# Kernel tuning notes

Hardware: AMD Instinct MI355X
Metric: run time of the kernel (lower is better)

The kernel has to match this reference:

```python
import jax, jax.numpy as jnp
import numpy as np

B, L, C, NEC = 1, 256, 1024, 2000


def setup_inputs() -> dict:
    key = jax.random.key(0)
    ks = jax.random.split(key, 8)
    attentions = jax.random.normal(ks[0], (B, L, C), jnp.float32)
    pooled = jax.random.normal(ks[1], (B, C), jnp.float32)
    attention_mask = jax.random.randint(ks[2], (B, L), 0, 2).astype(jnp.int32)
    lin1_w = jax.random.normal(ks[3], (C, C), jnp.float32) * 0.02
    lin1_b = jnp.zeros((C,), jnp.float32)
    cls_w = jax.random.normal(ks[4], (NEC, C), jnp.float32) * 0.02
    cls_b = jnp.zeros((NEC,), jnp.float32)
    conv1_w = jax.random.normal(ks[5], (C, 2 * C), jnp.float32) * 0.02  # 1x1 conv as matrix
    conv1_b = jnp.zeros((C,), jnp.float32)
    w2 = jax.random.normal(ks[6], (1, C, 7, 7), jnp.float32) * 0.02
    conv2_w = 0.5 * (w2 + jnp.swapaxes(w2, 2, 3))  # clip(): symmetrize kernel
    conv2_b = jnp.zeros((1,), jnp.float32)
    return dict(attentions=attentions, pooled=pooled, attention_mask=attention_mask,
                lin1_w=lin1_w, lin1_b=lin1_b, cls_w=cls_w, cls_b=cls_b,
                conv1_w=conv1_w, conv1_b=conv1_b, conv2_w=conv2_w, conv2_b=conv2_b)


def reference(attentions, pooled, attention_mask, lin1_w, lin1_b, cls_w, cls_b,
              conv1_w, conv1_b, conv2_w, conv2_b):
    # EC-classification head (dropout is identity at inference)
    logits = (pooled @ lin1_w.T + lin1_b) @ cls_w.T + cls_b  # [B, NEC]

    # mask out [CLS] (pos 0) and [SEP] (pos = sum of mask)
    s = attention_mask.sum(axis=1)
    mask = attention_mask.at[jnp.arange(B), s].set(0).at[:, 0].set(0)
    z = attentions * mask[:, :, None].astype(attentions.dtype)  # [B, L, C]
    z = jnp.swapaxes(z, 1, 2)                                   # [B, C, L]

    # pairwise |zi - zj| and zi * zj -> [B, 2C, L, L]
    z_diff = jnp.abs(z[:, :, None, :] - z[:, :, :, None])
    z_mul = z[:, :, None, :] * z[:, :, :, None]
    feat = jnp.concatenate([z_diff, z_mul], axis=1)

    # 1x1 conv (channel contraction) + ReLU
    h = jax.nn.relu(jnp.einsum('oc,bcij->boij', conv1_w, feat)
                    + conv1_b[None, :, None, None])            # [B, C, L, L]

    # 7x7 conv, padding 3, symmetric kernel, sigmoid
    out = jax.lax.conv_general_dilated(
        h, conv2_w, window_strides=(1, 1), padding=[(3, 3), (3, 3)],
        dimension_numbers=('NCHW', 'OIHW', 'NCHW')) + conv2_b[None, :, None, None]
    maps = jax.nn.sigmoid(out)                                  # [B, 1, L, L]
    return logits, maps.reshape(-1, L * L)
```

## Files before the change

### kernel.cpp

```cpp
#include <hip/hip_runtime.h>

typedef float  f4v    __attribute__((ext_vector_type(4)));
typedef __bf16 bf16x8 __attribute__((ext_vector_type(8)));
typedef __bf16 bf16x4 __attribute__((ext_vector_type(4)));

#define PCAP  16384
#define LDQ   16384
#define CH    1024
#define KI    2048
#define KIT   32

__device__ __forceinline__ int offA(int r, int A) { return r * A - ((r * (r - 1)) >> 1); }

__device__ __forceinline__ int mask_scan(const int* am, int t, int* act,
                                         unsigned long long* wm, int* wred) {
    int wave = t >> 6, lane = t & 63;
    int a = am[t];
    int sv = a;
#pragma unroll
    for (int d = 32; d; d >>= 1) sv += __shfl_down(sv, d);
    if (lane == 0) wred[wave] = sv;
    __syncthreads();
    int s = wred[0] + wred[1] + wred[2] + wred[3];
    int keep = (t != 0 && t != s && a != 0) ? 1 : 0;
    unsigned long long bm = __ballot(keep);
    if (lane == 0) wm[wave] = bm;
    __syncthreads();
    int base = 0, A = 0;
#pragma unroll
    for (int w = 0; w < 4; w++) {
        int pc = __popcll(wm[w]);
        if (w < wave) base += pc;
        A += pc;
    }
    if (keep) act[base + __popcll(bm & ((1ull << lane) - 1ull))] = t;
    __syncthreads();
    return A;
}

#define PB_FEATP  0
#define PB_FEATS  2048
#define PB_CVTA   2080
#define PB_K2     2592
#define PB_QCONST 2848
#define PB_ZERO   2897
#define PB_SCAN   3694
#define PB_HID    3695
#define PB_TOTAL  3951

__global__ void k_prep(const float* __restrict__ att, const int* __restrict__ am,
                       const float* __restrict__ c1w, const float* __restrict__ c2w,
                       const float* __restrict__ c1b,
                       const float* __restrict__ pooled, const float* __restrict__ lin1_w,
                       const float* __restrict__ lin1_b,
                       int* rank, int* counts, __bf16* featT, __bf16* A1p, __bf16* K2w,
                       float* Qc, float* Qzero, float* hid) {
    int b = blockIdx.x, t = threadIdx.x;

    if (b < PB_FEATS) {
        __shared__ int act[256];
        __shared__ unsigned long long wm[4];
        __shared__ int wred[4];
        int A = mask_scan(am, t, act, wm, wred);
        int P = (A * (A + 1)) >> 1;
        int Ppad = ((P + 127) >> 7) << 7;
        if (Ppad > PCAP) { Ppad = PCAP; P = PCAP; }
        int n0 = b * 8;
        if (n0 >= Ppad) return;
        int c0 = t * 4;
        float fA = (float)(2 * A + 1);
        for (int q = 0; q < 8; q++) {
            int n = n0 + q;
            bf16x8 ov;
            if (n < P && A > 0) {
                float disc = fmaxf(fA * fA - 8.0f * (float)n, 0.0f);
                int r = (int)floorf((fA - sqrtf(disc)) * 0.5f);
                r = min(A - 1, max(0, r));
                while (r > 0 && offA(r, A) > n) --r;
                while (r < A - 1 && offA(r + 1, A) <= n) ++r;
                int i = act[r], j = act[r + (n - offA(r, A))];
                float4 a = *(const float4*)&att[i * CH + c0];
                float4 bj = *(const float4*)&att[j * CH + c0];
                ov[0] = (__bf16)fabsf(a.x - bj.x); ov[1] = (__bf16)(a.x * bj.x);
                ov[2] = (__bf16)fabsf(a.y - bj.y); ov[3] = (__bf16)(a.y * bj.y);
                ov[4] = (__bf16)fabsf(a.z - bj.z); ov[5] = (__bf16)(a.z * bj.z);
                ov[6] = (__bf16)fabsf(a.w - bj.w); ov[7] = (__bf16)(a.w * bj.w);
            } else {
#pragma unroll
                for (int r8 = 0; r8 < 8; r8++) ov[r8] = (__bf16)0.0f;
            }
            *(bf16x8*)&featT[(size_t)n * KI + t * 8] = ov;
        }
    } else if (b < PB_CVTA) {
        int r0 = (b - PB_FEATS) * 8;
        int c0 = t * 4;
        for (int q = 0; q < 8; q++) {
            int r = r0 + q;
            float4 a = *(const float4*)&att[r * CH + c0];
            bf16x8 ov;
            ov[0] = (__bf16)fabsf(a.x); ov[1] = (__bf16)0.f;
            ov[2] = (__bf16)fabsf(a.y); ov[3] = (__bf16)0.f;
            ov[4] = (__bf16)fabsf(a.z); ov[5] = (__bf16)0.f;
            ov[6] = (__bf16)fabsf(a.w); ov[7] = (__bf16)0.f;
            *(bf16x8*)&featT[(size_t)(PCAP + r) * KI + t * 8] = ov;
        }
    } else if (b < PB_K2) {
        int gid = (b - PB_CVTA) * 256 + t;
        int o = gid >> 7, cw = (gid & 127) * 8;
        const float* wd = &c1w[o * 2048 + cw];
        const float* wmu = &c1w[o * 2048 + 1024 + cw];
        float4 d0 = *(const float4*)wd,  d1 = *(const float4*)(wd + 4);
        float4 m0 = *(const float4*)wmu, m1 = *(const float4*)(wmu + 4);
        bf16x8 v0, v1;
        v0[0] = (__bf16)d0.x; v0[1] = (__bf16)m0.x; v0[2] = (__bf16)d0.y; v0[3] = (__bf16)m0.y;
        v0[4] = (__bf16)d0.z; v0[5] = (__bf16)m0.z; v0[6] = (__bf16)d0.w; v0[7] = (__bf16)m0.w;
        v1[0] = (__bf16)d1.x; v1[1] = (__bf16)m1.x; v1[2] = (__bf16)d1.y; v1[3] = (__bf16)m1.y;
        v1[4] = (__bf16)d1.z; v1[5] = (__bf16)m1.z; v1[6] = (__bf16)d1.w; v1[7] = (__bf16)m1.w;
        *(bf16x8*)&A1p[o * 2048 + 2 * cw] = v0;
        *(bf16x8*)&A1p[o * 2048 + 2 * cw + 8] = v1;
    } else if (b < PB_QCONST) {
        int e = (b - PB_K2) * 256 + t;
        int trow = e >> 10, o = e & 1023;
        K2w[e] = (trow < 49) ? (__bf16)c2w[o * 49 + trow] : (__bf16)0.0f;
    } else if (b < PB_ZERO) {
        __shared__ float sh[256];
        int tap = b - PB_QCONST;
        float s = 0.f;
        for (int o = t; o < CH; o += 256) s += c2w[o * 49 + tap] * fmaxf(c1b[o], 0.f);
        sh[t] = s; __syncthreads();
        for (int d = 128; d; d >>= 1) { if (t < d) sh[t] += sh[t + d]; __syncthreads(); }
        if (t == 0) Qc[tap] = sh[0];
    } else if (b < PB_SCAN) {
        int idx = (b - PB_ZERO) * 256 + t;
        if (idx < 203840) {
            float4 zv = {0.f, 0.f, 0.f, 0.f};
            ((float4*)Qzero)[idx] = zv;
        }
    } else if (b == PB_SCAN) {
        __shared__ int act[256];
        __shared__ unsigned long long wm[4];
        __shared__ int wred[4];
        int A = mask_scan(am, t, act, wm, wred);
        int wave = t >> 6, lane = t & 63;
        int s = wred[0] + wred[1] + wred[2] + wred[3];
        int keep = (t != 0 && t != s && am[t] != 0) ? 1 : 0;
        int base = 0;
#pragma unroll
        for (int w = 0; w < 4; w++) if (w < wave) base += __popcll(wm[w]);
        unsigned long long bm = wm[wave];
        rank[t] = keep ? (base + __popcll(bm & ((1ull << lane) - 1ull))) : -1;
        if (t == 0) {
            int P = (A * (A + 1)) >> 1;
            int Pp = ((P + 127) >> 7) << 7;
            if (Pp > PCAP) Pp = PCAP;
            counts[0] = A; counts[1] = P; counts[2] = Pp;
        }
    } else {
        int o = (b - PB_HID) * 4 + (t >> 6);
        int lane = t & 63;
        const float* row = lin1_w + (size_t)o * CH;
        float s = 0.f;
        for (int c = lane; c < CH; c += 64) s += pooled[c] * row[c];
        for (int d = 32; d; d >>= 1) s += __shfl_down(s, d);
        if (lane == 0) hid[o] = s + lin1_b[o];
    }
}

__global__ __launch_bounds__(512) void gemm_fused(
        const __bf16* __restrict__ A1p, const __bf16* __restrict__ featT,
        const __bf16* __restrict__ K2w, const float* __restrict__ c1b,
        const int* __restrict__ counts,
        float* __restrict__ Q, float* __restrict__ Qs,
        const float* __restrict__ hid, const float* __restrict__ cls_w,
        const float* __restrict__ cls_b, float* __restrict__ logits) {
    int x = blockIdx.x, y = blockIdx.y;
    int tid = threadIdx.x, wave = tid >> 6, lane = tid & 63;

    if (x == 8) {
#pragma unroll
        for (int rr = 0; rr < 2; rr++) {
            int o = y * 16 + wave * 2 + rr;
            if (o >= 2000) break;
            const float* row = cls_w + (size_t)o * CH;
            float s = 0.f;
            for (int c = lane; c < CH; c += 64) s += hid[c] * row[c];
            for (int d = 32; d; d >>= 1) s += __shfl_down(s, d);
            if (lane == 0) logits[o] = s + cls_b[o];
        }
        return;
    }

    int Ppad = counts[2];
    int ntp = Ppad >> 7;
    int ntiles = ntp + 2;
    int c_rt = (ntiles + 7) >> 3;
    int g = (x + y) & 7;
    int nbl = y >> 3, mb = y & 7;
    if (nbl >= c_rt) return;
    int nb = g * c_rt + nbl;
    if (nb >= ntiles) return;
    bool sing = (nb >= ntp);
    int brow = sing ? (PCAP + (nb - ntp) * 128) : nb * 128;

    __shared__ __align__(16) char smemraw[65536];
#define ASP(bsel) ((__bf16(*)[64])(smemraw + (bsel) * 16384))
#define BSP(bsel) ((__bf16(*)[64])(smemraw + 32768 + (bsel) * 16384))
#define HTL ((__bf16(*)[136])(smemraw))
#define K2L ((__bf16(*)[136])(smemraw + 34816))

    int lanerow = lane >> 3;
    int swchunk = ((lane & 7) ^ lanerow) * 8;
    const __bf16* srcA = A1p + (size_t)(mb * 128 + wave * 16 + lanerow) * KI + swchunk;
    const __bf16* srcB = featT + (size_t)(brow + wave * 16 + lanerow) * KI + swchunk;

    f4v acc[4][2] = {};
    int row16 = lane & 15, quad = lane >> 4;
    int wx = wave & 3, wy = wave >> 2;

#define STAGE(kt, bsel)                                                           \
    {                                                                             \
        const __bf16* sA = srcA + (kt) * 64;                                      \
        _Pragma("unroll")                                                         \
        for (int q = 0; q < 2; q++) {                                             \
            __builtin_amdgcn_global_load_lds(                                     \
                (const __attribute__((address_space(1))) void*)(sA + (size_t)q * 8 * KI), \
                (__attribute__((address_space(3))) void*)&ASP(bsel)[wave * 16 + q * 8][0], 16, 0, 0); \
        }                                                                         \
        const __bf16* sB = srcB + (kt) * 64;                                      \
        _Pragma("unroll")                                                         \
        for (int q = 0; q < 2; q++) {                                             \
            __builtin_amdgcn_global_load_lds(                                     \
                (const __attribute__((address_space(1))) void*)(sB + (size_t)q * 8 * KI), \
                (__attribute__((address_space(3))) void*)&BSP(bsel)[wave * 16 + q * 8][0], 16, 0, 0); \
        }                                                                         \
    }

    STAGE(0, 0);
    for (int kt = 0; kt < KIT; ++kt) {
        int cur = kt & 1;
        if (kt + 1 < KIT) {
            STAGE(kt + 1, cur ^ 1);
            __builtin_amdgcn_s_waitcnt(0xF74);
        } else {
            __builtin_amdgcn_s_waitcnt(0xF70);
        }
        __builtin_amdgcn_s_barrier();
#pragma unroll
        for (int ks = 0; ks < 2; ks++) {
            bf16x8 a[4], b[2];
            int col = ((ks * 4 + quad) ^ (row16 & 7)) * 8;
#pragma unroll
            for (int mt = 0; mt < 4; mt++)
                a[mt] = *(const bf16x8*)&ASP(cur)[wy * 64 + mt * 16 + row16][col];
#pragma unroll
            for (int nt = 0; nt < 2; nt++)
                b[nt] = *(const bf16x8*)&BSP(cur)[wx * 32 + nt * 16 + row16][col];
#pragma unroll
            for (int mt = 0; mt < 4; mt++)
#pragma unroll
                for (int nt = 0; nt < 2; nt++)
                    acc[mt][nt] = __builtin_amdgcn_mfma_f32_16x16x32_bf16(a[mt], b[nt], acc[mt][nt], 0, 0, 0);
        }
        __builtin_amdgcn_s_barrier();
    }
#undef STAGE

#pragma unroll
    for (int it = 0; it < 2; it++) {
        int gid = it * 512 + tid;
        int trow = gid >> 4, oc = (gid & 15) * 8;
        bf16x8 kv = *(const bf16x8*)&K2w[(size_t)trow * CH + mb * 128 + oc];
        *(bf16x8*)&K2L[trow][oc] = kv;
    }
#pragma unroll
    for (int mt = 0; mt < 4; mt++) {
        int ol = wy * 64 + mt * 16 + quad * 4;
        float4 bv = *(const float4*)&c1b[mb * 128 + ol];
#pragma unroll
        for (int nt = 0; nt < 2; nt++) {
            int n = wx * 32 + nt * 16 + row16;
            bf16x4 pk;
            pk[0] = (__bf16)fmaxf(acc[mt][nt][0] + bv.x, 0.f);
            pk[1] = (__bf16)fmaxf(acc[mt][nt][1] + bv.y, 0.f);
            pk[2] = (__bf16)fmaxf(acc[mt][nt][2] + bv.z, 0.f);
            pk[3] = (__bf16)fmaxf(acc[mt][nt][3] + bv.w, 0.f);
            *(bf16x4*)&HTL[n][ol] = pk;
        }
    }
    __syncthreads();

    int tq = wave & 3, nhalf = wave >> 2;
    f4v acc2[4] = {};
#pragma unroll
    for (int ko = 0; ko < 4; ko++) {
        bf16x8 af = *(const bf16x8*)&K2L[tq * 16 + row16][ko * 32 + quad * 8];
#pragma unroll
        for (int nt = 0; nt < 4; nt++) {
            bf16x8 bf_ = *(const bf16x8*)&HTL[nhalf * 64 + nt * 16 + row16][ko * 32 + quad * 8];
            acc2[nt] = __builtin_amdgcn_mfma_f32_16x16x32_bf16(af, bf_, acc2[nt], 0, 0, 0);
        }
    }

    float* Qdst = sing ? Qs : Q;
    int ldq = sing ? 256 : LDQ;
    int nbase = sing ? (nb - ntp) * 128 : nb * 128;
    int t0 = tq * 16 + quad * 4;
#pragma unroll
    for (int nt = 0; nt < 4; nt++) {
        int n = nbase + nhalf * 64 + nt * 16 + row16;
#pragma unroll
        for (int r = 0; r < 4; r++)
            if (t0 + r < 49) atomicAdd(&Qdst[(size_t)(t0 + r) * ldq + n], acc2[nt][r]);
    }
#undef ASP
#undef BSP
#undef HTL
#undef K2L
}

__global__ void k_out(const float* __restrict__ Q, const float* __restrict__ Qs,
                      const float* __restrict__ Qc, const int* __restrict__ rank,
                      const int* __restrict__ counts, const float* b2,
                      float* __restrict__ outmaps) {
    __shared__ int rankL[256];
    __shared__ float QcL[49];
    int t = threadIdx.x, i = blockIdx.x;
    rankL[t] = rank[t];
    if (t < 49) QcL[t] = Qc[t];
    __syncthreads();
    int A = counts[0];
    int j = t;
    float acc = b2[0];
#pragma unroll
    for (int di = 0; di < 7; di++) {
        int p = i + di - 3;
        if ((unsigned)p > 255u) continue;
#pragma unroll
        for (int dj = 0; dj < 7; dj++) {
            int q = j + dj - 3;
            if ((unsigned)q > 255u) continue;
            int tt = di * 7 + dj;
            int a = min(p, q), bb = max(p, q);
            int ra = rankL[a], rb = rankL[bb];
            float val;
            if (ra >= 0) val = (rb >= 0) ? Q[(size_t)tt * LDQ + offA(ra, A) + (rb - ra)]
                                         : Qs[tt * 256 + a];
            else         val = (rb >= 0) ? Qs[tt * 256 + bb] : QcL[tt];
            acc += val;
        }
    }
    outmaps[i * 256 + j] = 1.0f / (1.0f + expf(-acc));
}


extern "C" void kernel_launch(void* const* d_in, const int* in_sizes, int n_in,
                              void* d_out, int out_size, void* d_ws, size_t ws_size,
                              hipStream_t stream) {
    const float* att    = (const float*)d_in[0];
    const float* pooled = (const float*)d_in[1];
    const int*   am     = (const int*)d_in[2];
    const float* lin1_w = (const float*)d_in[3];
    const float* lin1_b = (const float*)d_in[4];
    const float* cls_w  = (const float*)d_in[5];
    const float* cls_b  = (const float*)d_in[6];
    const float* c1w    = (const float*)d_in[7];
    const float* c1b    = (const float*)d_in[8];
    const float* c2w    = (const float*)d_in[9];
    const float* c2b    = (const float*)d_in[10];
    float* out = (float*)d_out;
    char*  ws  = (char*)d_ws;

    __bf16* A1p  = (__bf16*)(ws);
    __bf16* K2w  = (__bf16*)(ws + 4194304);
    float*  Q    = (float*) (ws + 4325376);
    float*  Qs   = (float*) (ws + 7536640);
    float*  Qc   = (float*) (ws + 7586816);
    int*    rank = (int*)   (ws + 7587072);
    float*  hid  = (float*) (ws + 7588096);
    int*    counts=(int*)   (ws + 7592192);
    __bf16* featT= (__bf16*)(ws + 7592960);

    k_prep<<<PB_TOTAL, 256, 0, stream>>>(att, am, c1w, c2w, c1b, pooled, lin1_w, lin1_b,
                                         rank, counts, featT, A1p, K2w, Qc, Q, hid);

    gemm_fused<<<dim3(9, 136), 512, 0, stream>>>(A1p, featT, K2w, c1b, counts, Q, Qs,
                                                 hid, cls_w, cls_b, out);

    k_out<<<256, 256, 0, stream>>>(Q, Qs, Qc, rank, counts, c2b, out + 2000);
}
```

Measured before the change: 158.3 us.

## Halve GEMM block to 4 waves with larger per-wave tiles; branchless output gather

The fused GEMM kernel moves from 8 waves to 4 waves per block. Each wave now computes a 64x64 output tile with 16 accumulators instead of 32x64, which raises MFMA-to-LDS-read reuse and halves the number of barrier participants. Staging loads per wave double, and the second-stage conv GEMM is remapped so each wave handles one 16-row tap slice across all 128 columns. Separately, k_out precomputes the per-column ranks and offsets and replaces its branchy gather with pointer selects and predicated accumulation, which trades some out-of-range clamped loads for less divergence. The larger tiles raise register pressure and reduce the number of waves available to hide latency.

Measured after the change: 160.1 us. Within noise of the previous version (+1.1%).

```diff
diff --git a/kernel.cpp b/kernel.cpp
--- a/kernel.cpp
+++ b/kernel.cpp
@@ -166,7 +166,7 @@
     }
 }
 
-__global__ __launch_bounds__(512) void gemm_fused(
+__global__ __launch_bounds__(256) void gemm_fused(
         const __bf16* __restrict__ A1p, const __bf16* __restrict__ featT,
         const __bf16* __restrict__ K2w, const float* __restrict__ c1b,
         const int* __restrict__ counts,
@@ -178,8 +178,8 @@
 
     if (x == 8) {
 #pragma unroll
-        for (int rr = 0; rr < 2; rr++) {
-            int o = y * 16 + wave * 2 + rr;
+        for (int rr = 0; rr < 4; rr++) {
+            int o = y * 16 + wave * 4 + rr;
             if (o >= 2000) break;
             const float* row = cls_w + (size_t)o * CH;
             float s = 0.f;
@@ -210,28 +210,28 @@
 
     int lanerow = lane >> 3;
     int swchunk = ((lane & 7) ^ lanerow) * 8;
-    const __bf16* srcA = A1p + (size_t)(mb * 128 + wave * 16 + lanerow) * KI + swchunk;
-    const __bf16* srcB = featT + (size_t)(brow + wave * 16 + lanerow) * KI + swchunk;
-
-    f4v acc[4][2] = {};
+    const __bf16* srcA = A1p + (size_t)(mb * 128 + wave * 32 + lanerow) * KI + swchunk;
+    const __bf16* srcB = featT + (size_t)(brow + wave * 32 + lanerow) * KI + swchunk;
+
+    f4v acc[4][4] = {};
     int row16 = lane & 15, quad = lane >> 4;
-    int wx = wave & 3, wy = wave >> 2;
+    int wx = wave & 1, wy = wave >> 1;
 
 #define STAGE(kt, bsel)                                                           \
     {                                                                             \
         const __bf16* sA = srcA + (kt) * 64;                                      \
         _Pragma("unroll")                                                         \
-        for (int q = 0; q < 2; q++) {                                             \
+        for (int q = 0; q < 4; q++) {                                             \
             __builtin_amdgcn_global_load_lds(                                     \
                 (const __attribute__((address_space(1))) void*)(sA + (size_t)q * 8 * KI), \
-                (__attribute__((address_space(3))) void*)&ASP(bsel)[wave * 16 + q * 8][0], 16, 0, 0); \
+                (__attribute__((address_space(3))) void*)&ASP(bsel)[wave * 32 + q * 8][0], 16, 0, 0); \
         }                                                                         \
         const __bf16* sB = srcB + (kt) * 64;                                      \
         _Pragma("unroll")                                                         \
-        for (int q = 0; q < 2; q++) {                                             \
+        for (int q = 0; q < 4; q++) {                                             \
             __builtin_amdgcn_global_load_lds(                                     \
                 (const __attribute__((address_space(1))) void*)(sB + (size_t)q * 8 * KI), \
-                (__attribute__((address_space(3))) void*)&BSP(bsel)[wave * 16 + q * 8][0], 16, 0, 0); \
+                (__attribute__((address_space(3))) void*)&BSP(bsel)[wave * 32 + q * 8][0], 16, 0, 0); \
         }                                                                         \
     }
 
@@ -240,25 +240,25 @@
         int cur = kt & 1;
         if (kt + 1 < KIT) {
             STAGE(kt + 1, cur ^ 1);
-            __builtin_amdgcn_s_waitcnt(0xF74);
+            __builtin_amdgcn_s_waitcnt(0xF78);
         } else {
             __builtin_amdgcn_s_waitcnt(0xF70);
         }
         __builtin_amdgcn_s_barrier();
 #pragma unroll
         for (int ks = 0; ks < 2; ks++) {
-            bf16x8 a[4], b[2];
+            bf16x8 a[4], b[4];
             int col = ((ks * 4 + quad) ^ (row16 & 7)) * 8;
 #pragma unroll
             for (int mt = 0; mt < 4; mt++)
                 a[mt] = *(const bf16x8*)&ASP(cur)[wy * 64 + mt * 16 + row16][col];
 #pragma unroll
-            for (int nt = 0; nt < 2; nt++)
-                b[nt] = *(const bf16x8*)&BSP(cur)[wx * 32 + nt * 16 + row16][col];
+            for (int nt = 0; nt < 4; nt++)
+                b[nt] = *(const bf16x8*)&BSP(cur)[wx * 64 + nt * 16 + row16][col];
 #pragma unroll
             for (int mt = 0; mt < 4; mt++)
 #pragma unroll
-                for (int nt = 0; nt < 2; nt++)
+                for (int nt = 0; nt < 4; nt++)
                     acc[mt][nt] = __builtin_amdgcn_mfma_f32_16x16x32_bf16(a[mt], b[nt], acc[mt][nt], 0, 0, 0);
         }
         __builtin_amdgcn_s_barrier();
@@ -266,8 +266,8 @@
 #undef STAGE
 
 #pragma unroll
-    for (int it = 0; it < 2; it++) {
-        int gid = it * 512 + tid;
+    for (int it = 0; it < 4; it++) {
+        int gid = it * 256 + tid;
         int trow = gid >> 4, oc = (gid & 15) * 8;
         bf16x8 kv = *(const bf16x8*)&K2w[(size_t)trow * CH + mb * 128 + oc];
         *(bf16x8*)&K2L[trow][oc] = kv;
@@ -277,8 +277,8 @@
         int ol = wy * 64 + mt * 16 + quad * 4;
         float4 bv = *(const float4*)&c1b[mb * 128 + ol];
 #pragma unroll
-        for (int nt = 0; nt < 2; nt++) {
-            int n = wx * 32 + nt * 16 + row16;
+        for (int nt = 0; nt < 4; nt++) {
+            int n = wx * 64 + nt * 16 + row16;
             bf16x4 pk;
             pk[0] = (__bf16)fmaxf(acc[mt][nt][0] + bv.x, 0.f);
             pk[1] = (__bf16)fmaxf(acc[mt][nt][1] + bv.y, 0.f);
@@ -289,14 +289,13 @@
     }
     __syncthreads();
 
-    int tq = wave & 3, nhalf = wave >> 2;
-    f4v acc2[4] = {};
+    f4v acc2[8] = {};
 #pragma unroll
     for (int ko = 0; ko < 4; ko++) {
-        bf16x8 af = *(const bf16x8*)&K2L[tq * 16 + row16][ko * 32 + quad * 8];
-#pragma unroll
-        for (int nt = 0; nt < 4; nt++) {
-            bf16x8 bf_ = *(const bf16x8*)&HTL[nhalf * 64 + nt * 16 + row16][ko * 32 + quad * 8];
+        bf16x8 af = *(const bf16x8*)&K2L[wave * 16 + row16][ko * 32 + quad * 8];
+#pragma unroll
+        for (int nt = 0; nt < 8; nt++) {
+            bf16x8 bf_ = *(const bf16x8*)&HTL[nt * 16 + row16][ko * 32 + quad * 8];
             acc2[nt] = __builtin_amdgcn_mfma_f32_16x16x32_bf16(af, bf_, acc2[nt], 0, 0, 0);
         }
     }
@@ -304,10 +303,10 @@
     float* Qdst = sing ? Qs : Q;
     int ldq = sing ? 256 : LDQ;
     int nbase = sing ? (nb - ntp) * 128 : nb * 128;
-    int t0 = tq * 16 + quad * 4;
-#pragma unroll
-    for (int nt = 0; nt < 4; nt++) {
-        int n = nbase + nhalf * 64 + nt * 16 + row16;
+    int t0 = wave * 16 + quad * 4;
+#pragma unroll
+    for (int nt = 0; nt < 8; nt++) {
+        int n = nbase + nt * 16 + row16;
 #pragma unroll
         for (int r = 0; r < 4; r++)
             if (t0 + r < 49) atomicAdd(&Qdst[(size_t)(t0 + r) * ldq + n], acc2[nt][r]);
@@ -323,30 +322,50 @@
                       const int* __restrict__ counts, const float* b2,
                       float* __restrict__ outmaps) {
     __shared__ int rankL[256];
-    __shared__ float QcL[49];
     int t = threadIdx.x, i = blockIdx.x;
     rankL[t] = rank[t];
-    if (t < 49) QcL[t] = Qc[t];
     __syncthreads();
     int A = counts[0];
     int j = t;
+
+    int qc_[7], rq_[7], oq_[7];
+    bool vq_[7];
+#pragma unroll
+    for (int dj = 0; dj < 7; dj++) {
+        int q = j + dj - 3;
+        vq_[dj] = ((unsigned)q <= 255u);
+        int qc = min(255, max(0, q));
+        qc_[dj] = qc;
+        int r = rankL[qc];
+        rq_[dj] = r;
+        oq_[dj] = offA(max(r, 0), A);
+    }
+
     float acc = b2[0];
 #pragma unroll
     for (int di = 0; di < 7; di++) {
         int p = i + di - 3;
-        if ((unsigned)p > 255u) continue;
+        bool vp = ((unsigned)p <= 255u);
+        int pc = min(255, max(0, p));
+        int rp = rankL[pc];
+        int op = offA(max(rp, 0), A);
 #pragma unroll
         for (int dj = 0; dj < 7; dj++) {
-            int q = j + dj - 3;
-            if ((unsigned)q > 255u) continue;
             int tt = di * 7 + dj;
-            int a = min(p, q), bb = max(p, q);
-            int ra = rankL[a], rb = rankL[bb];
-            float val;
-            if (ra >= 0) val = (rb >= 0) ? Q[(size_t)tt * LDQ + offA(ra, A) + (rb - ra)]
-                                         : Qs[tt * 256 + a];
-            else         val = (rb >= 0) ? Qs[tt * 256 + bb] : QcL[tt];
-            acc += val;
+            int qc = qc_[dj];
+            bool pfirst = (pc <= qc);
+            int a  = pfirst ? pc : qc;
+            int bb = pfirst ? qc : pc;
+            int ra = pfirst ? rp : rq_[dj];
+            int rb = pfirst ? rq_[dj] : rp;
+            int oa = pfirst ? op : oq_[dj];
+            const float* s1 = (rb >= 0) ? (Q + (size_t)tt * LDQ + (oa + rb - ra))
+                                        : (Qs + tt * 256 + a);
+            const float* s0 = (rb >= 0) ? (Qs + tt * 256 + bb)
+                                        : (Qc + tt);
+            const float* sp = (ra >= 0) ? s1 : s0;
+            float val = *sp;
+            acc = (vp && vq_[dj]) ? (acc + val) : acc;
         }
     }
     outmaps[i * 256 + j] = 1.0f / (1.0f + expf(-acc));
@@ -383,7 +402,7 @@
     k_prep<<<PB_TOTAL, 256, 0, stream>>>(att, am, c1w, c2w, c1b, pooled, lin1_w, lin1_b,
                                          rank, counts, featT, A1p, K2w, Qc, Q, hid);
 
-    gemm_fused<<<dim3(9, 136), 512, 0, stream>>>(A1p, featT, K2w, c1b, counts, Q, Qs,
+    gemm_fused<<<dim3(9, 136), 256, 0, stream>>>(A1p, featT, K2w, c1b, counts, Q, Qs,
                                                  hid, cls_w, cls_b, out);
 
     k_out<<<256, 256, 0, stream>>>(Q, Qs, Qc, rank, counts, c2b, out + 2000);
```
